# Kernel tuning notes

Measured on AMD Instinct MI355X. Metric: run time of the kernel, lower is better.

Reference implementation:

```python
import jax, jax.numpy as jnp
import numpy as np

HIDDEN = 1024
HEADS = 16
D_K = HIDDEN // HEADS
B, S = 2, 2048


def setup_inputs() -> dict:
    key = jax.random.key(0)
    ks = jax.random.split(key, 11)
    sc = 1.0 / np.sqrt(HIDDEN)
    return {
        "query": jax.random.normal(ks[0], (B, S, HIDDEN), jnp.float32),
        "key": jax.random.normal(ks[1], (B, S, HIDDEN), jnp.float32),
        "value": jax.random.normal(ks[2], (B, S, HIDDEN), jnp.float32),
        "w_q": jax.random.normal(ks[3], (HIDDEN, HIDDEN), jnp.float32) * sc,
        "b_q": jax.random.normal(ks[4], (HIDDEN,), jnp.float32) * 0.02,
        "w_k": jax.random.normal(ks[5], (HIDDEN, HIDDEN), jnp.float32) * sc,
        "b_k": jax.random.normal(ks[6], (HIDDEN,), jnp.float32) * 0.02,
        "w_v": jax.random.normal(ks[7], (HIDDEN, HIDDEN), jnp.float32) * sc,
        "b_v": jax.random.normal(ks[8], (HIDDEN,), jnp.float32) * 0.02,
        "w_o": jax.random.normal(ks[9], (HIDDEN, HIDDEN), jnp.float32) * sc,
        "b_o": jax.random.normal(ks[10], (HIDDEN,), jnp.float32) * 0.02,
    }


def reference(query, key, value, w_q, b_q, w_k, b_k, w_v, b_v, w_o, b_o):
    b, s, _ = query.shape
    # linear projections (torch Linear: x @ W^T + b)
    q = query @ w_q.T + b_q
    k = key @ w_k.T + b_k
    v = value @ w_v.T + b_v
    # [B, H, S, D]
    q = q.reshape(b, s, HEADS, D_K).transpose(0, 2, 1, 3)
    k = k.reshape(b, s, HEADS, D_K).transpose(0, 2, 1, 3)
    v = v.reshape(b, s, HEADS, D_K).transpose(0, 2, 1, 3)
    scale = jnp.float32(1.0 / np.sqrt(D_K))
    scores = jnp.einsum('bhqd,bhkd->bhqk', q, k) * scale  # [B,H,S,S]
    probs = jax.nn.softmax(scores, axis=-1)
    y = jnp.einsum('bhqk,bhkd->bhqd', probs, v)
    y = y.transpose(0, 2, 1, 3).reshape(b, s, HIDDEN)
    return y @ w_o.T + b_o
```

## Files before the change

### kernel.cpp

```cpp
#include <hip/hip_runtime.h>
#include <hip/hip_bf16.h>
#include <math.h>

#define HIDDEN 1024
#define HEADS 16
#define DK 64
#define BB 2
#define SS 2048
#define MROWS (BB*SS)

typedef __attribute__((ext_vector_type(8))) short short8;
typedef __attribute__((ext_vector_type(4))) float f32x4;
typedef __attribute__((ext_vector_type(16))) float f32x16;
typedef __attribute__((ext_vector_type(4))) unsigned short ushort4_t;

static __device__ __forceinline__ unsigned short f2bf(float f) {
    unsigned int u = __float_as_uint(f);
    u += 0x7fffu + ((u >> 16) & 1u);
    return (unsigned short)(u >> 16);
}
static __device__ __forceinline__ float bf2f(unsigned short s) {
    return __uint_as_float(((unsigned int)s) << 16);
}

static __device__ __forceinline__ unsigned int cvtpk(float lo, float hi) {
    unsigned int r;
    asm volatile("v_cvt_pk_bf16_f32 %0, %1, %2" : "=v"(r) : "v"(lo), "v"(hi));
    return r;
}
static __device__ __forceinline__ void swap32(unsigned int& a, unsigned int& b) {
    asm volatile("v_permlane32_swap_b32 %0, %1" : "+v"(a), "+v"(b));
}
static __device__ __forceinline__ short8 pack_bf16x8(float4 lo, float4 hi) {
    union { unsigned int u[4]; short8 s; } r;
    r.u[0] = cvtpk(lo.x, lo.y);
    r.u[1] = cvtpk(lo.z, lo.w);
    r.u[2] = cvtpk(hi.x, hi.y);
    r.u[3] = cvtpk(hi.z, hi.w);
    return r.s;
}

__global__ __launch_bounds__(256) void cast_all(
    const float* __restrict__ q, const float* __restrict__ k, const float* __restrict__ v,
    const float* __restrict__ wq, const float* __restrict__ wk, const float* __restrict__ wv,
    unsigned short* __restrict__ Xq, unsigned short* __restrict__ Xk, unsigned short* __restrict__ Xv,
    unsigned short* __restrict__ Wq, unsigned short* __restrict__ Wk, unsigned short* __restrict__ Wv) {
    int i = blockIdx.x * 256 + threadIdx.x;
    const float* src; unsigned short* dst; int off;
    if (i < (3 << 20)) {
        int w = i >> 20; off = i & ((1 << 20) - 1);
        src = (w == 0) ? q : (w == 1) ? k : v;
        dst = (w == 0) ? Xq : (w == 1) ? Xk : Xv;
    } else {
        int j = i - (3 << 20);
        int w = j >> 18; off = j & ((1 << 18) - 1);
        src = (w == 0) ? wq : (w == 1) ? wk : wv;
        dst = (w == 0) ? Wq : (w == 1) ? Wk : Wv;
    }
    float4 f = reinterpret_cast<const float4*>(src)[off];
    ushort4_t o;
    o.x = f2bf(f.x); o.y = f2bf(f.y); o.z = f2bf(f.z); o.w = f2bf(f.w);
    reinterpret_cast<ushort4_t*>(dst)[off] = o;
}

__global__ __launch_bounds__(256, 4) void gemm_qkv(
    const unsigned short* __restrict__ Xq, const unsigned short* __restrict__ Xk, const unsigned short* __restrict__ Xv,
    const unsigned short* __restrict__ Wq, const unsigned short* __restrict__ Wk, const unsigned short* __restrict__ Wv,
    const float* __restrict__ bq, const float* __restrict__ bk, const float* __restrict__ bv,
    unsigned short* __restrict__ Qb, unsigned short* __restrict__ Kb, unsigned short* __restrict__ Vt,
    float scale_q) {
    __shared__ __attribute__((aligned(16))) unsigned short As[128 * 64];
    __shared__ __attribute__((aligned(16))) unsigned short Bs[128 * 64];
    const int lid = blockIdx.x + 8 * (blockIdx.y + 32 * blockIdx.z);
    const int c = lid & 7, i2 = lid >> 3;
    const int nb = i2 & 7;
    const int band = c * 12 + (i2 >> 3);
    const int yb = band & 31;
    const int z  = band >> 5;
    const unsigned short* A  = (z == 0) ? Xq : (z == 1) ? Xk : Xv;
    const unsigned short* Wt = (z == 0) ? Wq : (z == 1) ? Wk : Wv;
    const float* bias = (z == 0) ? bq : (z == 1) ? bk : bv;
    unsigned short* O = (z == 0) ? Qb : (z == 1) ? Kb : Vt;
    const float oscale = (z == 0) ? scale_q : 1.0f;

    const int t    = threadIdx.x;
    const int lane = t & 63;
    const int wave = t >> 6;
    const int m0 = yb * 128;
    const int n0 = nb * 128;

    const int wm = (wave >> 1) * 64;
    const int wn = (wave & 1) * 64;
    const int lr = lane & 15;
    const int g  = lane >> 4;
    const int sr = lane >> 3;
    const int cs = (lane & 7) ^ sr;

    f32x4 acc[4][4];
#pragma unroll
    for (int i = 0; i < 4; i++)
#pragma unroll
        for (int j = 0; j < 4; j++) acc[i][j] = f32x4{0.f, 0.f, 0.f, 0.f};

#define GSTAGE(K0) do {                                                                      \
    _Pragma("unroll")                                                                        \
    for (int jj = 0; jj < 4; jj++) {                                                         \
        int rb = wave * 32 + jj * 8;                                                         \
        __builtin_amdgcn_global_load_lds(                                                    \
            (const __attribute__((address_space(1))) unsigned int*)(A + (size_t)(m0 + rb + sr) * HIDDEN + (K0) + cs * 8), \
            (__attribute__((address_space(3))) unsigned int*)&As[rb * 64], 16, 0, 0);        \
        __builtin_amdgcn_global_load_lds(                                                    \
            (const __attribute__((address_space(1))) unsigned int*)(Wt + (size_t)(n0 + rb + sr) * HIDDEN + (K0) + cs * 8), \
            (__attribute__((address_space(3))) unsigned int*)&Bs[rb * 64], 16, 0, 0);        \
    }                                                                                        \
} while (0)

    for (int k0 = 0; k0 < HIDDEN; k0 += 64) {
        GSTAGE(k0);
        __syncthreads();
#pragma unroll
        for (int kk = 0; kk < 2; kk++) {
            short8 af[4], bfr[4];
#pragma unroll
            for (int i = 0; i < 4; i++)
                af[i] = *reinterpret_cast<const short8*>(
                    &As[(wm + i * 16 + lr) * 64 + (((kk * 4 + g) ^ (lr & 7)) << 3)]);
#pragma unroll
            for (int j = 0; j < 4; j++)
                bfr[j] = *reinterpret_cast<const short8*>(
                    &Bs[(wn + j * 16 + lr) * 64 + (((kk * 4 + g) ^ (lr & 7)) << 3)]);
#pragma unroll
            for (int i = 0; i < 4; i++)
#pragma unroll
                for (int j = 0; j < 4; j++)
                    acc[i][j] = __builtin_amdgcn_mfma_f32_16x16x32_bf16(af[i], bfr[j], acc[i][j], 0, 0, 0);
        }
        __syncthreads();
    }
#undef GSTAGE

#pragma unroll
    for (int i = 0; i < 4; i++) {
        int mrow = m0 + wm + i * 16 + (lane >> 4) * 4;
#pragma unroll
        for (int j = 0; j < 4; j++) {
            int ncol = n0 + wn + j * 16 + lr;
            float bvv = bias[ncol];
            int b_ = mrow >> 11;
            int h_ = ncol >> 6;
            int d_ = ncol & 63;
            if (z != 2) {
#pragma unroll
                for (int r = 0; r < 4; r++) {
                    int s_ = (mrow + r) & 2047;
                    O[(((size_t)(b_ * HEADS + h_)) * SS + s_) * DK + d_] = f2bf((acc[i][j][r] + bvv) * oscale);
                }
            } else {
                int s0 = mrow & 2047;
                ushort4_t pk;
                pk.x = f2bf(acc[i][j][0] + bvv);
                pk.y = f2bf(acc[i][j][1] + bvv);
                pk.z = f2bf(acc[i][j][2] + bvv);
                pk.w = f2bf(acc[i][j][3] + bvv);
                *reinterpret_cast<ushort4_t*>(O + (((size_t)(b_ * HEADS + h_) * DK + d_) * SS + s0)) = pk;
            }
        }
    }
}

__global__ __launch_bounds__(256) void gemm_o(const unsigned short* __restrict__ A,
                                              const float* __restrict__ Wt,
                                              const float* __restrict__ bias,
                                              float* __restrict__ O) {
    __shared__ unsigned short As[128][40];
    __shared__ unsigned short Bs[64][40];
    const int lid = blockIdx.x + 16 * blockIdx.y;
    const int c = lid & 7, i2 = lid >> 3;
    const int nb = i2 & 15;
    const int band = c * 4 + (i2 >> 4);
    const int t    = threadIdx.x;
    const int lane = t & 63;
    const int wave = t >> 6;
    const int m0 = band * 128;
    const int n0 = nb * 64;
    const int row  = t >> 2;
    const int col8 = (t & 3) * 8;

    const int wm = wave * 32;
    const int lr = lane & 15;
    const int lk = (lane >> 4) * 8;

    f32x4 acc[2][4];
#pragma unroll
    for (int i = 0; i < 2; i++)
#pragma unroll
        for (int j = 0; j < 4; j++) acc[i][j] = f32x4{0.f, 0.f, 0.f, 0.f};

    for (int k0 = 0; k0 < HIDDEN; k0 += 32) {
        short8 av0 = *reinterpret_cast<const short8*>(A + (size_t)(m0 + row)      * HIDDEN + k0 + col8);
        short8 av1 = *reinterpret_cast<const short8*>(A + (size_t)(m0 + row + 64) * HIDDEN + k0 + col8);
        const float* w0 = Wt + (size_t)(n0 + row) * HIDDEN + k0 + col8;
        float4 w00 = reinterpret_cast<const float4*>(w0)[0];
        float4 w01 = reinterpret_cast<const float4*>(w0)[1];
        __syncthreads();
        *reinterpret_cast<short8*>(&As[row][col8])      = av0;
        *reinterpret_cast<short8*>(&As[row + 64][col8]) = av1;
        *reinterpret_cast<short8*>(&Bs[row][col8])      = pack_bf16x8(w00, w01);
        __syncthreads();
        short8 af[2], bfr[4];
#pragma unroll
        for (int i = 0; i < 2; i++) af[i]  = *reinterpret_cast<const short8*>(&As[wm + i * 16 + lr][lk]);
#pragma unroll
        for (int j = 0; j < 4; j++) bfr[j] = *reinterpret_cast<const short8*>(&Bs[j * 16 + lr][lk]);
#pragma unroll
        for (int i = 0; i < 2; i++)
#pragma unroll
            for (int j = 0; j < 4; j++)
                acc[i][j] = __builtin_amdgcn_mfma_f32_16x16x32_bf16(af[i], bfr[j], acc[i][j], 0, 0, 0);
    }

#pragma unroll
    for (int i = 0; i < 2; i++) {
        int mrow = m0 + wm + i * 16 + (lane >> 4) * 4;
#pragma unroll
        for (int j = 0; j < 4; j++) {
            int ncol = n0 + j * 16 + lr;
            float bvv = bias[ncol];
#pragma unroll
            for (int r = 0; r < 4; r++)
                O[(size_t)(mrow + r) * HIDDEN + ncol] = acc[i][j][r] + bvv;
        }
    }
}

__global__ __launch_bounds__(256, 4) void attn_kernel(const unsigned short* __restrict__ Qb,
                                                      const unsigned short* __restrict__ Kb,
                                                      const unsigned short* __restrict__ Vt,
                                                      unsigned short* __restrict__ Yb0,
                                                      unsigned short* __restrict__ Yb1,
                                                      float* __restrict__ ml) {
    __shared__ __attribute__((aligned(16))) unsigned short Ksh[2][64 * 64];
    __shared__ __attribute__((aligned(16))) unsigned short Vsh[2][64 * 64];
    __shared__ float Lsh[4][32];

    const int t    = threadIdx.x;
    const int lane = t & 63;
    const int wave = t >> 6;
    const int fid  = blockIdx.x;
    const int c    = fid & 7;
    const int i    = fid >> 3;
    const int qblk = i & 15;
    const int pair = c * 8 + (i >> 4);
    const int bh   = pair >> 1;
    const int kvh  = pair & 1;
    const int b_ = bh >> 4, h_ = bh & 15;
    const int qbase = qblk * 128 + wave * 32;
    const int kvbase = kvh << 10;
    const unsigned short* Qp = Qb + (size_t)bh * SS * DK;
    const unsigned short* Kp = Kb + (size_t)bh * SS * DK;
    const unsigned short* Vp = Vt + (size_t)bh * DK * SS;
    const int lq = lane & 31;
    const int hi = lane >> 5;
    const int sr = lane >> 3;
    const int cs = (lane & 7) ^ sr;

    short8 qf[4];
#pragma unroll
    for (int cc = 0; cc < 4; cc++)
        qf[cc] = *reinterpret_cast<const short8*>(Qp + (size_t)(qbase + lq) * DK + cc * 16 + hi * 8);

    f32x16 acc0, acc1;
#pragma unroll
    for (int r = 0; r < 16; r++) { acc0[r] = 0.f; acc1[r] = 0.f; }
    float li = 0.f;

#define STAGE(BUF, KV0) do {                                                                 \
    __builtin_amdgcn_global_load_lds(                                                        \
        (const __attribute__((address_space(1))) unsigned int*)(Kp + (size_t)((KV0) + wave * 16 + sr) * DK + cs * 8), \
        (__attribute__((address_space(3))) unsigned int*)&Ksh[BUF][(wave * 16) * 64], 16, 0, 0); \
    __builtin_amdgcn_global_load_lds(                                                        \
        (const __attribute__((address_space(1))) unsigned int*)(Kp + (size_t)((KV0) + wave * 16 + 8 + sr) * DK + cs * 8), \
        (__attribute__((address_space(3))) unsigned int*)&Ksh[BUF][(wave * 16 + 8) * 64], 16, 0, 0); \
    __builtin_amdgcn_global_load_lds(                                                        \
        (const __attribute__((address_space(1))) unsigned int*)(Vp + (size_t)(wave * 16 + sr) * SS + (KV0) + cs * 8), \
        (__attribute__((address_space(3))) unsigned int*)&Vsh[BUF][(wave * 16) * 64], 16, 0, 0); \
    __builtin_amdgcn_global_load_lds(                                                        \
        (const __attribute__((address_space(1))) unsigned int*)(Vp + (size_t)(wave * 16 + 8 + sr) * SS + (KV0) + cs * 8), \
        (__attribute__((address_space(3))) unsigned int*)&Vsh[BUF][(wave * 16 + 8) * 64], 16, 0, 0); \
} while (0)

    STAGE(0, kvbase);
    __syncthreads();

    for (int kv0 = kvbase; kv0 < kvbase + 1024; kv0 += 64) {
        const int cur = (kv0 >> 6) & 1;
        if (kv0 + 64 < kvbase + 1024) STAGE(cur ^ 1, kv0 + 64);

        f32x16 sv0, sv1;
#pragma unroll
        for (int r = 0; r < 16; r++) { sv0[r] = 0.f; sv1[r] = 0.f; }
#pragma unroll
        for (int cc = 0; cc < 4; cc++) {
            short8 kf0 = *reinterpret_cast<const short8*>(
                &Ksh[cur][lq * 64 + (((2 * cc + hi) ^ (lq & 7)) << 3)]);
            short8 kf1 = *reinterpret_cast<const short8*>(
                &Ksh[cur][(32 + lq) * 64 + (((2 * cc + hi) ^ (lq & 7)) << 3)]);
            sv0 = __builtin_amdgcn_mfma_f32_32x32x16_bf16(kf0, qf[cc], sv0, 0, 0, 0);
            sv1 = __builtin_amdgcn_mfma_f32_32x32x16_bf16(kf1, qf[cc], sv1, 0, 0, 0);
        }

        float pt[2][16];
        float rs = 0.f;
#pragma unroll
        for (int r = 0; r < 16; r++) {
            pt[0][r] = __builtin_amdgcn_exp2f(sv0[r] - 32.0f);
            pt[1][r] = __builtin_amdgcn_exp2f(sv1[r] - 32.0f);
            rs += pt[0][r] + pt[1][r];
        }
        rs += __shfl_xor(rs, 32);
        li += rs;

        short8 fragP[4];
#pragma unroll
        for (int tt = 0; tt < 2; tt++)
#pragma unroll
            for (int cl = 0; cl < 2; cl++) {
                unsigned int w0 = cvtpk(pt[tt][cl * 8 + 0], pt[tt][cl * 8 + 1]);
                unsigned int w1 = cvtpk(pt[tt][cl * 8 + 2], pt[tt][cl * 8 + 3]);
                unsigned int w2 = cvtpk(pt[tt][cl * 8 + 4], pt[tt][cl * 8 + 5]);
                unsigned int w3 = cvtpk(pt[tt][cl * 8 + 6], pt[tt][cl * 8 + 7]);
                swap32(w0, w2);
                swap32(w1, w3);
                union { unsigned int u[4]; short8 s; } f;
                f.u[0] = w0; f.u[1] = w1; f.u[2] = w2; f.u[3] = w3;
                fragP[tt * 2 + cl] = f.s;
            }

#pragma unroll
        for (int cc = 0; cc < 4; cc++) {
            short8 vf0 = *reinterpret_cast<const short8*>(
                &Vsh[cur][lq * 64 + (((2 * cc + hi) ^ (lq & 7)) << 3)]);
            short8 vf1 = *reinterpret_cast<const short8*>(
                &Vsh[cur][(32 + lq) * 64 + (((2 * cc + hi) ^ (lq & 7)) << 3)]);
            acc0 = __builtin_amdgcn_mfma_f32_32x32x16_bf16(fragP[cc], vf0, acc0, 0, 0, 0);
            acc1 = __builtin_amdgcn_mfma_f32_32x32x16_bf16(fragP[cc], vf1, acc1, 0, 0, 0);
        }
        __syncthreads();
    }
#undef STAGE

    unsigned short* Yp = kvh ? Yb1 : Yb0;
    if (lane < 32) {
        Lsh[wave][lq] = 1.0f / li;
        ml[(((size_t)kvh * 32 + bh) << 11) + qbase + lq] = li;
    }
    __syncthreads();
#pragma unroll
    for (int r = 0; r < 16; r++) {
        int qr = (r & 3) + 8 * (r >> 2) + 4 * hi;
        float inv = Lsh[wave][qr];
        size_t base = ((size_t)b_ * SS + qbase + qr) * HIDDEN + h_ * 64 + lq;
        Yp[base]      = f2bf(acc0[r] * inv);
        Yp[base + 32] = f2bf(acc1[r] * inv);
    }
}

__global__ __launch_bounds__(256) void combine_halves(const unsigned short* __restrict__ Yb0,
                                                      const unsigned short* __restrict__ Yb1,
                                                      const float* __restrict__ ml,
                                                      unsigned short* __restrict__ Yb) {
    int j = blockIdx.x * 256 + threadIdx.x;
    int chunk = j & 127;
    int s = (j >> 7) & 2047;
    int b = j >> 18;
    int h = chunk >> 3;
    int bh = b * 16 + h;
    float l0 = ml[((size_t)bh << 11) + s];
    float l1 = ml[(((size_t)32 + bh) << 11) + s];
    float inv = 1.0f / (l0 + l1);
    float w0 = l0 * inv, w1 = l1 * inv;
    short8 a = reinterpret_cast<const short8*>(Yb0)[j];
    short8 bb = reinterpret_cast<const short8*>(Yb1)[j];
    union { unsigned int u[4]; short8 s8; } o;
#pragma unroll
    for (int k = 0; k < 4; k++) {
        float lo = w0 * bf2f((unsigned short)a[2 * k])     + w1 * bf2f((unsigned short)bb[2 * k]);
        float hi = w0 * bf2f((unsigned short)a[2 * k + 1]) + w1 * bf2f((unsigned short)bb[2 * k + 1]);
        o.u[k] = cvtpk(lo, hi);
    }
    reinterpret_cast<short8*>(Yb)[j] = o.s8;
}

extern "C" void kernel_launch(void* const* d_in, const int* in_sizes, int n_in,
                              void* d_out, int out_size, void* d_ws, size_t ws_size,
                              hipStream_t stream) {
    const float* query = (const float*)d_in[0];
    const float* key_  = (const float*)d_in[1];
    const float* value = (const float*)d_in[2];
    const float* w_q = (const float*)d_in[3];
    const float* b_q = (const float*)d_in[4];
    const float* w_k = (const float*)d_in[5];
    const float* b_k = (const float*)d_in[6];
    const float* w_v = (const float*)d_in[7];
    const float* b_v = (const float*)d_in[8];
    const float* w_o = (const float*)d_in[9];
    const float* b_o = (const float*)d_in[10];

    const size_t SZ_X = (size_t)MROWS * HIDDEN * 2;
    const size_t SZ_W = (size_t)HIDDEN * HIDDEN * 2;
    char* ws = (char*)d_ws;
    unsigned short* Xq = (unsigned short*)(ws);
    unsigned short* Xk = (unsigned short*)(ws + SZ_X);
    unsigned short* Xv = (unsigned short*)(ws + 2 * SZ_X);
    unsigned short* Wq = (unsigned short*)(ws + 3 * SZ_X);
    unsigned short* Wk = (unsigned short*)(ws + 3 * SZ_X + SZ_W);
    unsigned short* Wv = (unsigned short*)(ws + 3 * SZ_X + 2 * SZ_W);
    unsigned short* Qb  = (unsigned short*)(ws + 3 * SZ_X + 3 * SZ_W);
    unsigned short* Kbf = (unsigned short*)(ws + 4 * SZ_X + 3 * SZ_W);
    unsigned short* Vt  = (unsigned short*)(ws + 5 * SZ_X + 3 * SZ_W);
    unsigned short* Yb0 = (unsigned short*)(ws + 6 * SZ_X + 3 * SZ_W);
    unsigned short* Yb1 = (unsigned short*)(ws + 7 * SZ_X + 3 * SZ_W);
    unsigned short* Yb  = (unsigned short*)(ws + 8 * SZ_X + 3 * SZ_W);
    float*          ml  = (float*)(ws + 9 * SZ_X + 3 * SZ_W);

    cast_all<<<15360, 256, 0, stream>>>(query, key_, value, w_q, w_k, w_v,
                                        Xq, Xk, Xv, Wq, Wk, Wv);

    const float SCALE_Q = 0.125f * 1.4426950408889634f;
    gemm_qkv<<<dim3(8, 32, 3), 256, 0, stream>>>(
        Xq, Xk, Xv, Wq, Wk, Wv, b_q, b_k, b_v, Qb, Kbf, Vt, SCALE_Q);

    attn_kernel<<<dim3(1024), 256, 0, stream>>>(Qb, Kbf, Vt, Yb0, Yb1, ml);

    combine_halves<<<dim3(2048), 256, 0, stream>>>(Yb0, Yb1, ml, Yb);

    gemm_o<<<dim3(16, 32), 256, 0, stream>>>(Yb, w_o, b_o, (float*)d_out);
}
```

Baseline: 127.3 us.

## Fuse activation fp32-to-bf16 cast into QKV GEMM and add MFMA priority hints

Drops the separate cast pass over the query/key/value activations. The QKV GEMM now loads fp32 tiles straight into LDS with a swizzle and converts them to bf16 when building fragments, which removes a full read-write round trip of the activations. The cost is a doubled A-tile LDS footprint, extra conversion instructions inside the GEMM loop, and a lower occupancy hint (3 instead of 4). Separately, the attention kernel wraps its MFMA blocks in s_setprio raises to favour matrix issue over other waves.

```diff
diff --git a/kernel.cpp b/kernel.cpp
--- a/kernel.cpp
+++ b/kernel.cpp
@@ -40,36 +40,26 @@
     return r.s;
 }
 
-__global__ __launch_bounds__(256) void cast_all(
-    const float* __restrict__ q, const float* __restrict__ k, const float* __restrict__ v,
+__global__ __launch_bounds__(256) void cast_w(
     const float* __restrict__ wq, const float* __restrict__ wk, const float* __restrict__ wv,
-    unsigned short* __restrict__ Xq, unsigned short* __restrict__ Xk, unsigned short* __restrict__ Xv,
     unsigned short* __restrict__ Wq, unsigned short* __restrict__ Wk, unsigned short* __restrict__ Wv) {
     int i = blockIdx.x * 256 + threadIdx.x;
-    const float* src; unsigned short* dst; int off;
-    if (i < (3 << 20)) {
-        int w = i >> 20; off = i & ((1 << 20) - 1);
-        src = (w == 0) ? q : (w == 1) ? k : v;
-        dst = (w == 0) ? Xq : (w == 1) ? Xk : Xv;
-    } else {
-        int j = i - (3 << 20);
-        int w = j >> 18; off = j & ((1 << 18) - 1);
-        src = (w == 0) ? wq : (w == 1) ? wk : wv;
-        dst = (w == 0) ? Wq : (w == 1) ? Wk : Wv;
-    }
+    int w = i >> 18, off = i & ((1 << 18) - 1);
+    const float* src = (w == 0) ? wq : (w == 1) ? wk : wv;
+    unsigned short* dst = (w == 0) ? Wq : (w == 1) ? Wk : Wv;
     float4 f = reinterpret_cast<const float4*>(src)[off];
     ushort4_t o;
     o.x = f2bf(f.x); o.y = f2bf(f.y); o.z = f2bf(f.z); o.w = f2bf(f.w);
     reinterpret_cast<ushort4_t*>(dst)[off] = o;
 }
 
-__global__ __launch_bounds__(256, 4) void gemm_qkv(
-    const unsigned short* __restrict__ Xq, const unsigned short* __restrict__ Xk, const unsigned short* __restrict__ Xv,
+__global__ __launch_bounds__(256, 3) void gemm_qkv(
+    const float* __restrict__ Xq, const float* __restrict__ Xk, const float* __restrict__ Xv,
     const unsigned short* __restrict__ Wq, const unsigned short* __restrict__ Wk, const unsigned short* __restrict__ Wv,
     const float* __restrict__ bq, const float* __restrict__ bk, const float* __restrict__ bv,
     unsigned short* __restrict__ Qb, unsigned short* __restrict__ Kb, unsigned short* __restrict__ Vt,
     float scale_q) {
-    __shared__ __attribute__((aligned(16))) unsigned short As[128 * 64];
+    __shared__ __attribute__((aligned(16))) float Asf[128 * 64];
     __shared__ __attribute__((aligned(16))) unsigned short Bs[128 * 64];
     const int lid = blockIdx.x + 8 * (blockIdx.y + 32 * blockIdx.z);
     const int c = lid & 7, i2 = lid >> 3;
@@ -77,7 +67,7 @@
     const int band = c * 12 + (i2 >> 3);
     const int yb = band & 31;
     const int z  = band >> 5;
-    const unsigned short* A  = (z == 0) ? Xq : (z == 1) ? Xk : Xv;
+    const float* A           = (z == 0) ? Xq : (z == 1) ? Xk : Xv;
     const unsigned short* Wt = (z == 0) ? Wq : (z == 1) ? Wk : Wv;
     const float* bias = (z == 0) ? bq : (z == 1) ? bk : bv;
     unsigned short* O = (z == 0) ? Qb : (z == 1) ? Kb : Vt;
@@ -93,8 +83,9 @@
     const int wn = (wave & 1) * 64;
     const int lr = lane & 15;
     const int g  = lane >> 4;
-    const int sr = lane >> 3;
-    const int cs = (lane & 7) ^ sr;
+    const int sr  = lane >> 3;
+    const int cs8 = (lane & 7) ^ sr;
+    const int ar  = lane >> 4;
 
     f32x4 acc[4][4];
 #pragma unroll
@@ -103,14 +94,19 @@
         for (int j = 0; j < 4; j++) acc[i][j] = f32x4{0.f, 0.f, 0.f, 0.f};
 
 #define GSTAGE(K0) do {                                                                      \
+    _Pragma("unroll")                                                                        \
+    for (int jj = 0; jj < 8; jj++) {                                                         \
+        int rb = wave * 32 + jj * 4;                                                         \
+        int csa = (lane & 15) ^ ((rb + ar) & 15);                                            \
+        __builtin_amdgcn_global_load_lds(                                                    \
+            (const __attribute__((address_space(1))) unsigned int*)(A + (size_t)(m0 + rb + ar) * HIDDEN + (K0) + csa * 4), \
+            (__attribute__((address_space(3))) unsigned int*)&Asf[rb * 64], 16, 0, 0);       \
+    }                                                                                        \
     _Pragma("unroll")                                                                        \
     for (int jj = 0; jj < 4; jj++) {                                                         \
         int rb = wave * 32 + jj * 8;                                                         \
         __builtin_amdgcn_global_load_lds(                                                    \
-            (const __attribute__((address_space(1))) unsigned int*)(A + (size_t)(m0 + rb + sr) * HIDDEN + (K0) + cs * 8), \
-            (__attribute__((address_space(3))) unsigned int*)&As[rb * 64], 16, 0, 0);        \
-        __builtin_amdgcn_global_load_lds(                                                    \
-            (const __attribute__((address_space(1))) unsigned int*)(Wt + (size_t)(n0 + rb + sr) * HIDDEN + (K0) + cs * 8), \
+            (const __attribute__((address_space(1))) unsigned int*)(Wt + (size_t)(n0 + rb + sr) * HIDDEN + (K0) + cs8 * 8), \
             (__attribute__((address_space(3))) unsigned int*)&Bs[rb * 64], 16, 0, 0);        \
     }                                                                                        \
 } while (0)
@@ -122,9 +118,13 @@
         for (int kk = 0; kk < 2; kk++) {
             short8 af[4], bfr[4];
 #pragma unroll
-            for (int i = 0; i < 4; i++)
-                af[i] = *reinterpret_cast<const short8*>(
-                    &As[(wm + i * 16 + lr) * 64 + (((kk * 4 + g) ^ (lr & 7)) << 3)]);
+            for (int i = 0; i < 4; i++) {
+                int row = wm + i * 16 + lr;
+                int cg = kk * 8 + g * 2;
+                float4 a0 = *reinterpret_cast<const float4*>(&Asf[row * 64 + ((cg     ^ lr) << 2)]);
+                float4 a1 = *reinterpret_cast<const float4*>(&Asf[row * 64 + (((cg + 1) ^ lr) << 2)]);
+                af[i] = pack_bf16x8(a0, a1);
+            }
 #pragma unroll
             for (int j = 0; j < 4; j++)
                 bfr[j] = *reinterpret_cast<const short8*>(
@@ -299,6 +299,7 @@
         f32x16 sv0, sv1;
 #pragma unroll
         for (int r = 0; r < 16; r++) { sv0[r] = 0.f; sv1[r] = 0.f; }
+        __builtin_amdgcn_s_setprio(1);
 #pragma unroll
         for (int cc = 0; cc < 4; cc++) {
             short8 kf0 = *reinterpret_cast<const short8*>(
@@ -308,6 +309,7 @@
             sv0 = __builtin_amdgcn_mfma_f32_32x32x16_bf16(kf0, qf[cc], sv0, 0, 0, 0);
             sv1 = __builtin_amdgcn_mfma_f32_32x32x16_bf16(kf1, qf[cc], sv1, 0, 0, 0);
         }
+        __builtin_amdgcn_s_setprio(0);
 
         float pt[2][16];
         float rs = 0.f;
@@ -336,6 +338,7 @@
                 fragP[tt * 2 + cl] = f.s;
             }
 
+        __builtin_amdgcn_s_setprio(1);
 #pragma unroll
         for (int cc = 0; cc < 4; cc++) {
             short8 vf0 = *reinterpret_cast<const short8*>(
@@ -345,6 +348,7 @@
             acc0 = __builtin_amdgcn_mfma_f32_32x32x16_bf16(fragP[cc], vf0, acc0, 0, 0, 0);
             acc1 = __builtin_amdgcn_mfma_f32_32x32x16_bf16(fragP[cc], vf1, acc1, 0, 0, 0);
         }
+        __builtin_amdgcn_s_setprio(0);
         __syncthreads();
     }
 #undef STAGE
@@ -409,26 +413,22 @@
     const size_t SZ_X = (size_t)MROWS * HIDDEN * 2;
     const size_t SZ_W = (size_t)HIDDEN * HIDDEN * 2;
     char* ws = (char*)d_ws;
-    unsigned short* Xq = (unsigned short*)(ws);
-    unsigned short* Xk = (unsigned short*)(ws + SZ_X);
-    unsigned short* Xv = (unsigned short*)(ws + 2 * SZ_X);
-    unsigned short* Wq = (unsigned short*)(ws + 3 * SZ_X);
-    unsigned short* Wk = (unsigned short*)(ws + 3 * SZ_X + SZ_W);
-    unsigned short* Wv = (unsigned short*)(ws + 3 * SZ_X + 2 * SZ_W);
-    unsigned short* Qb  = (unsigned short*)(ws + 3 * SZ_X + 3 * SZ_W);
-    unsigned short* Kbf = (unsigned short*)(ws + 4 * SZ_X + 3 * SZ_W);
-    unsigned short* Vt  = (unsigned short*)(ws + 5 * SZ_X + 3 * SZ_W);
-    unsigned short* Yb0 = (unsigned short*)(ws + 6 * SZ_X + 3 * SZ_W);
-    unsigned short* Yb1 = (unsigned short*)(ws + 7 * SZ_X + 3 * SZ_W);
-    unsigned short* Yb  = (unsigned short*)(ws + 8 * SZ_X + 3 * SZ_W);
-    float*          ml  = (float*)(ws + 9 * SZ_X + 3 * SZ_W);
-
-    cast_all<<<15360, 256, 0, stream>>>(query, key_, value, w_q, w_k, w_v,
-                                        Xq, Xk, Xv, Wq, Wk, Wv);
+    unsigned short* Wq = (unsigned short*)(ws);
+    unsigned short* Wk = (unsigned short*)(ws + SZ_W);
+    unsigned short* Wv = (unsigned short*)(ws + 2 * SZ_W);
+    unsigned short* Qb  = (unsigned short*)(ws + 3 * SZ_W);
+    unsigned short* Kbf = (unsigned short*)(ws + 3 * SZ_W + SZ_X);
+    unsigned short* Vt  = (unsigned short*)(ws + 3 * SZ_W + 2 * SZ_X);
+    unsigned short* Yb0 = (unsigned short*)(ws + 3 * SZ_W + 3 * SZ_X);
+    unsigned short* Yb1 = (unsigned short*)(ws + 3 * SZ_W + 4 * SZ_X);
+    unsigned short* Yb  = (unsigned short*)(ws + 3 * SZ_W + 5 * SZ_X);
+    float*          ml  = (float*)(ws + 3 * SZ_W + 6 * SZ_X);
+
+    cast_w<<<3072, 256, 0, stream>>>(w_q, w_k, w_v, Wq, Wk, Wv);
 
     const float SCALE_Q = 0.125f * 1.4426950408889634f;
     gemm_qkv<<<dim3(8, 32, 3), 256, 0, stream>>>(
-        Xq, Xk, Xv, Wq, Wk, Wv, b_q, b_k, b_v, Qb, Kbf, Vt, SCALE_Q);
+        query, key_, value, Wq, Wk, Wv, b_q, b_k, b_v, Qb, Kbf, Vt, SCALE_Q);
 
     attn_kernel<<<dim3(1024), 256, 0, stream>>>(Qb, Kbf, Vt, Yb0, Yb1, ml);
 
```

Measured after the change: 124.7 us. 1.02x faster.

## Fuse split-KV half combination into output projection and raise MFMA priority

Applied to the files above, without the earlier changes.

The separate combine_halves kernel, which merged the two split-KV attention partial outputs using their softmax sums, is removed. That merge now runs inside gemm_o's A-tile load: each thread reads both partial bf16 tiles and the ml sums, then weights, combines and packs the values before writing them to LDS. This saves a kernel launch and a full write and read of the intermediate Yb buffer. In exchange, gemm_o does twice the A loads plus the divisions, repeated once per N-block (16 times per row). The attention kernel also wraps its MFMA loops in s_setprio to favour matrix issue.

```diff
diff --git a/kernel.cpp b/kernel.cpp
--- a/kernel.cpp
+++ b/kernel.cpp
@@ -30,14 +30,6 @@
 }
 static __device__ __forceinline__ void swap32(unsigned int& a, unsigned int& b) {
     asm volatile("v_permlane32_swap_b32 %0, %1" : "+v"(a), "+v"(b));
-}
-static __device__ __forceinline__ short8 pack_bf16x8(float4 lo, float4 hi) {
-    union { unsigned int u[4]; short8 s; } r;
-    r.u[0] = cvtpk(lo.x, lo.y);
-    r.u[1] = cvtpk(lo.z, lo.w);
-    r.u[2] = cvtpk(hi.x, hi.y);
-    r.u[3] = cvtpk(hi.z, hi.w);
-    return r.s;
 }
 
 __global__ __launch_bounds__(256) void cast_all(
@@ -168,7 +160,9 @@
     }
 }
 
-__global__ __launch_bounds__(256) void gemm_o(const unsigned short* __restrict__ A,
+__global__ __launch_bounds__(256) void gemm_o(const unsigned short* __restrict__ Yb0,
+                                              const unsigned short* __restrict__ Yb1,
+                                              const float* __restrict__ ml,
                                               const float* __restrict__ Wt,
                                               const float* __restrict__ bias,
                                               float* __restrict__ O) {
@@ -197,15 +191,41 @@
         for (int j = 0; j < 4; j++) acc[i][j] = f32x4{0.f, 0.f, 0.f, 0.f};
 
     for (int k0 = 0; k0 < HIDDEN; k0 += 32) {
-        short8 av0 = *reinterpret_cast<const short8*>(A + (size_t)(m0 + row)      * HIDDEN + k0 + col8);
-        short8 av1 = *reinterpret_cast<const short8*>(A + (size_t)(m0 + row + 64) * HIDDEN + k0 + col8);
+        int h = (k0 + col8) >> 6;
+        short8 a0r0 = *reinterpret_cast<const short8*>(Yb0 + (size_t)(m0 + row)      * HIDDEN + k0 + col8);
+        short8 a1r0 = *reinterpret_cast<const short8*>(Yb1 + (size_t)(m0 + row)      * HIDDEN + k0 + col8);
+        short8 a0r1 = *reinterpret_cast<const short8*>(Yb0 + (size_t)(m0 + row + 64) * HIDDEN + k0 + col8);
+        short8 a1r1 = *reinterpret_cast<const short8*>(Yb1 + (size_t)(m0 + row + 64) * HIDDEN + k0 + col8);
+        int mr0 = m0 + row, mr1 = m0 + row + 64;
+        int bh0 = (mr0 >> 11) * 16 + h, s0 = mr0 & 2047;
+        int bh1 = (mr1 >> 11) * 16 + h, s1 = mr1 & 2047;
+        float l00 = ml[((size_t)bh0 << 11) + s0];
+        float l01 = ml[(((size_t)32 + bh0) << 11) + s0];
+        float l10 = ml[((size_t)bh1 << 11) + s1];
+        float l11 = ml[(((size_t)32 + bh1) << 11) + s1];
+        float iv0 = 1.0f / (l00 + l01), w00 = l00 * iv0, w01 = l01 * iv0;
+        float iv1 = 1.0f / (l10 + l11), w10 = l10 * iv1, w11 = l11 * iv1;
         const float* w0 = Wt + (size_t)(n0 + row) * HIDDEN + k0 + col8;
-        float4 w00 = reinterpret_cast<const float4*>(w0)[0];
-        float4 w01 = reinterpret_cast<const float4*>(w0)[1];
+        float4 ww0 = reinterpret_cast<const float4*>(w0)[0];
+        float4 ww1 = reinterpret_cast<const float4*>(w0)[1];
+        union { unsigned int u[4]; short8 s8; } cr0, cr1, wpk;
+#pragma unroll
+        for (int kq = 0; kq < 4; kq++) {
+            float lo0 = w00 * bf2f((unsigned short)a0r0[2 * kq])     + w01 * bf2f((unsigned short)a1r0[2 * kq]);
+            float hi0 = w00 * bf2f((unsigned short)a0r0[2 * kq + 1]) + w01 * bf2f((unsigned short)a1r0[2 * kq + 1]);
+            cr0.u[kq] = cvtpk(lo0, hi0);
+            float lo1 = w10 * bf2f((unsigned short)a0r1[2 * kq])     + w11 * bf2f((unsigned short)a1r1[2 * kq]);
+            float hi1 = w10 * bf2f((unsigned short)a0r1[2 * kq + 1]) + w11 * bf2f((unsigned short)a1r1[2 * kq + 1]);
+            cr1.u[kq] = cvtpk(lo1, hi1);
+        }
+        wpk.u[0] = cvtpk(ww0.x, ww0.y);
+        wpk.u[1] = cvtpk(ww0.z, ww0.w);
+        wpk.u[2] = cvtpk(ww1.x, ww1.y);
+        wpk.u[3] = cvtpk(ww1.z, ww1.w);
         __syncthreads();
-        *reinterpret_cast<short8*>(&As[row][col8])      = av0;
-        *reinterpret_cast<short8*>(&As[row + 64][col8]) = av1;
-        *reinterpret_cast<short8*>(&Bs[row][col8])      = pack_bf16x8(w00, w01);
+        *reinterpret_cast<short8*>(&As[row][col8])      = cr0.s8;
+        *reinterpret_cast<short8*>(&As[row + 64][col8]) = cr1.s8;
+        *reinterpret_cast<short8*>(&Bs[row][col8])      = wpk.s8;
         __syncthreads();
         short8 af[2], bfr[4];
 #pragma unroll
@@ -299,6 +319,7 @@
         f32x16 sv0, sv1;
 #pragma unroll
         for (int r = 0; r < 16; r++) { sv0[r] = 0.f; sv1[r] = 0.f; }
+        __builtin_amdgcn_s_setprio(1);
 #pragma unroll
         for (int cc = 0; cc < 4; cc++) {
             short8 kf0 = *reinterpret_cast<const short8*>(
@@ -308,6 +329,7 @@
             sv0 = __builtin_amdgcn_mfma_f32_32x32x16_bf16(kf0, qf[cc], sv0, 0, 0, 0);
             sv1 = __builtin_amdgcn_mfma_f32_32x32x16_bf16(kf1, qf[cc], sv1, 0, 0, 0);
         }
+        __builtin_amdgcn_s_setprio(0);
 
         float pt[2][16];
         float rs = 0.f;
@@ -336,6 +358,7 @@
                 fragP[tt * 2 + cl] = f.s;
             }
 
+        __builtin_amdgcn_s_setprio(1);
 #pragma unroll
         for (int cc = 0; cc < 4; cc++) {
             short8 vf0 = *reinterpret_cast<const short8*>(
@@ -345,6 +368,7 @@
             acc0 = __builtin_amdgcn_mfma_f32_32x32x16_bf16(fragP[cc], vf0, acc0, 0, 0, 0);
             acc1 = __builtin_amdgcn_mfma_f32_32x32x16_bf16(fragP[cc], vf1, acc1, 0, 0, 0);
         }
+        __builtin_amdgcn_s_setprio(0);
         __syncthreads();
     }
 #undef STAGE
@@ -363,32 +387,6 @@
         Yp[base]      = f2bf(acc0[r] * inv);
         Yp[base + 32] = f2bf(acc1[r] * inv);
     }
-}
-
-__global__ __launch_bounds__(256) void combine_halves(const unsigned short* __restrict__ Yb0,
-                                                      const unsigned short* __restrict__ Yb1,
-                                                      const float* __restrict__ ml,
-                                                      unsigned short* __restrict__ Yb) {
-    int j = blockIdx.x * 256 + threadIdx.x;
-    int chunk = j & 127;
-    int s = (j >> 7) & 2047;
-    int b = j >> 18;
-    int h = chunk >> 3;
-    int bh = b * 16 + h;
-    float l0 = ml[((size_t)bh << 11) + s];
-    float l1 = ml[(((size_t)32 + bh) << 11) + s];
-    float inv = 1.0f / (l0 + l1);
-    float w0 = l0 * inv, w1 = l1 * inv;
-    short8 a = reinterpret_cast<const short8*>(Yb0)[j];
-    short8 bb = reinterpret_cast<const short8*>(Yb1)[j];
-    union { unsigned int u[4]; short8 s8; } o;
-#pragma unroll
-    for (int k = 0; k < 4; k++) {
-        float lo = w0 * bf2f((unsigned short)a[2 * k])     + w1 * bf2f((unsigned short)bb[2 * k]);
-        float hi = w0 * bf2f((unsigned short)a[2 * k + 1]) + w1 * bf2f((unsigned short)bb[2 * k + 1]);
-        o.u[k] = cvtpk(lo, hi);
-    }
-    reinterpret_cast<short8*>(Yb)[j] = o.s8;
 }
 
 extern "C" void kernel_launch(void* const* d_in, const int* in_sizes, int n_in,
@@ -420,8 +418,7 @@
     unsigned short* Vt  = (unsigned short*)(ws + 5 * SZ_X + 3 * SZ_W);
     unsigned short* Yb0 = (unsigned short*)(ws + 6 * SZ_X + 3 * SZ_W);
     unsigned short* Yb1 = (unsigned short*)(ws + 7 * SZ_X + 3 * SZ_W);
-    unsigned short* Yb  = (unsigned short*)(ws + 8 * SZ_X + 3 * SZ_W);
-    float*          ml  = (float*)(ws + 9 * SZ_X + 3 * SZ_W);
+    float*          ml  = (float*)(ws + 8 * SZ_X + 3 * SZ_W);
 
     cast_all<<<15360, 256, 0, stream>>>(query, key_, value, w_q, w_k, w_v,
                                         Xq, Xk, Xv, Wq, Wk, Wv);
@@ -432,7 +429,5 @@
 
     attn_kernel<<<dim3(1024), 256, 0, stream>>>(Qb, Kbf, Vt, Yb0, Yb1, ml);
 
-    combine_halves<<<dim3(2048), 256, 0, stream>>>(Yb0, Yb1, ml, Yb);
-
-    gemm_o<<<dim3(16, 32), 256, 0, stream>>>(Yb, w_o, b_o, (float*)d_out);
-}
+    gemm_o<<<dim3(16, 32), 256, 0, stream>>>(Yb0, Yb1, ml, w_o, b_o, (float*)d_out);
+}
```

New measurement: 141.7 us. 11.3% more time.
